# Kernel tuning notes

Hardware: AMD Instinct MI355X
Metric: run time of the kernel (lower is better)

The kernel has to match this reference:

```python
import jax, jax.numpy as jnp
import numpy as np

N = 50000      # nodes
E = 800000     # edges (avg degree 16)
D = 128        # feature / channel width (channel_counts=[128,128,128])
HEAD = 64      # head_dim
NEG_SLOPE = 0.2  # PyG GATConv leaky_relu slope


def setup_inputs() -> dict:
    key = jax.random.key(0)
    ks = jax.random.split(key, 32)
    s = 1.0 / np.sqrt(D)

    def w(k, shape):
        return jax.random.normal(k, shape, jnp.float32) * s

    return {
        "x": jax.random.normal(ks[0], (N, D), jnp.float32),
        "edge_index": jax.random.randint(ks[1], (2, E), 0, N, dtype=jnp.int32),
        # layer 0: lazy (-1,-1) GATConv -> separate src/dst linear maps
        "w0_src": w(ks[2], (D, D)), "w0_dst": w(ks[3], (D, D)),
        "a0_src": w(ks[4], (D,)), "a0_dst": w(ks[5], (D,)),
        "bc0": jnp.zeros((D,), jnp.float32),
        "wl0": w(ks[6], (D, D)), "bl0": jnp.zeros((D,), jnp.float32),
        # layer 1: int in_channels -> shared weight
        "w1": w(ks[7], (D, D)),
        "a1_src": w(ks[8], (D,)), "a1_dst": w(ks[9], (D,)),
        "bc1": jnp.zeros((D,), jnp.float32),
        "wl1": w(ks[10], (D, D)), "bl1": jnp.zeros((D,), jnp.float32),
        # layer 2
        "w2": w(ks[11], (D, D)),
        "a2_src": w(ks[12], (D,)), "a2_dst": w(ks[13], (D,)),
        "bc2": jnp.zeros((D,), jnp.float32),
        "wl2": w(ks[14], (D, D)), "bl2": jnp.zeros((D,), jnp.float32),
        # head linear
        "wh": w(ks[15], (D, HEAD)), "bh": jnp.zeros((HEAD,), jnp.float32),
    }


def _gat(h_src, h_dst, src, dst, a_src, a_dst, bias):
    """PyG GATConv (heads=1, no self loops, eval-mode). h_*: [N,C]."""
    al_s = h_src @ a_src                                   # [N]
    al_d = h_dst @ a_dst                                   # [N]
    logits = jax.nn.leaky_relu(al_s[src] + al_d[dst], NEG_SLOPE)  # [E]
    m = jax.ops.segment_max(logits, dst, num_segments=N)  # per-dest max
    e = jnp.exp(logits - m[dst])
    denom = jax.ops.segment_sum(e, dst, num_segments=N)
    alpha = e / denom[dst]                                 # [E]
    msg = h_src[src] * alpha[:, None]                      # [E,C]
    return jax.ops.segment_sum(msg, dst, num_segments=N) + bias


def reference(x, edge_index, w0_src, w0_dst, a0_src, a0_dst, bc0, wl0, bl0,
              w1, a1_src, a1_dst, bc1, wl1, bl1,
              w2, a2_src, a2_dst, bc2, wl2, bl2, wh, bh):
    src, dst = edge_index[0], edge_index[1]
    # layer 0: conv(x) + lin(x), relu
    h = _gat(x @ w0_src, x @ w0_dst, src, dst, a0_src, a0_dst, bc0) + x @ wl0 + bl0
    h = jax.nn.relu(h)
    # layer 1: shared-weight conv
    hs = h @ w1
    h = _gat(hs, hs, src, dst, a1_src, a1_dst, bc1) + h @ wl1 + bl1
    h = jax.nn.relu(h)
    # layer 2 (no relu)
    hs = h @ w2
    h = _gat(hs, hs, src, dst, a2_src, a2_dst, bc2) + h @ wl2 + bl2
    # head
    return h @ wh + bh
```

## Files before the change

kernel.cpp:

```cpp
#include <hip/hip_runtime.h>

#define NNODE 50000
#define NEDGE 800000
#define DIM   128
#define NEG   0.2f
#define NBUCK 196
#define EPB1  2048
#define NB1   391
#define GBLK  782

typedef __attribute__((ext_vector_type(8))) short bf16x8;
typedef __attribute__((ext_vector_type(4))) float f32x4;

__device__ __forceinline__ float wmax(float v){
  #pragma unroll
  for (int m = 32; m > 0; m >>= 1) v = fmaxf(v, __shfl_xor(v, m));
  return v;
}
__device__ __forceinline__ float wsum(float v){
  #pragma unroll
  for (int m = 32; m > 0; m >>= 1) v += __shfl_xor(v, m);
  return v;
}
__device__ __forceinline__ unsigned short f2bf(float f){
  unsigned int x = __float_as_uint(f);
  return (unsigned short)((x + 0x7fffu + ((x >> 16) & 1u)) >> 16);
}
__device__ __forceinline__ float bflo(unsigned u){ return __uint_as_float(u << 16); }
__device__ __forceinline__ float bfhi(unsigned u){ return __uint_as_float(u & 0xffff0000u); }

__global__ __launch_bounds__(256) void bhist2_k(const int* __restrict__ dst,
                                                int* __restrict__ cnt){
  __shared__ int h[NBUCK];
  for (int i = threadIdx.x; i < NBUCK; i += 256) h[i] = 0;
  __syncthreads();
  int e0 = blockIdx.x * EPB1 + threadIdx.x;
  #pragma unroll
  for (int i = 0; i < 8; ++i){
    int e = e0 + i * 256;
    if (e < NEDGE) atomicAdd(&h[dst[e] >> 8], 1);
  }
  __syncthreads();
  for (int i = threadIdx.x; i < NBUCK; i += 256)
    cnt[i * NB1 + blockIdx.x] = h[i];
}

__global__ __launch_bounds__(256) void scan196_k(const int* __restrict__ cnt,
                                                 int* __restrict__ cbase,
                                                 int* __restrict__ btot){
  __shared__ int sd[256];
  int b = blockIdx.x, t = threadIdx.x;
  const int* row = cnt + (size_t)b * NB1;
  int i0 = t * 2, i1 = t * 2 + 1;
  int v0 = (i0 < NB1) ? row[i0] : 0;
  int v1 = (i1 < NB1) ? row[i1] : 0;
  int s = v0 + v1;
  sd[t] = s; __syncthreads();
  #pragma unroll
  for (int off = 1; off < 256; off <<= 1){
    int u = (t >= off) ? sd[t - off] : 0;
    __syncthreads();
    sd[t] += u;
    __syncthreads();
  }
  int ex = sd[t] - s;
  if (i0 < NB1) cbase[(size_t)b * NB1 + i0] = ex;
  if (i1 < NB1) cbase[(size_t)b * NB1 + i1] = ex + v0;
  if (t == 255) btot[b] = sd[255];
}

__global__ __launch_bounds__(256) void bscan2_k(const int* __restrict__ btot,
                                                int* __restrict__ gbase,
                                                int* __restrict__ rp){
  __shared__ int sd[256];
  int t = threadIdx.x;
  int v = (t < NBUCK) ? btot[t] : 0;
  sd[t] = v; __syncthreads();
  #pragma unroll
  for (int off = 1; off < 256; off <<= 1){
    int u = (t >= off) ? sd[t - off] : 0;
    __syncthreads();
    sd[t] += u;
    __syncthreads();
  }
  if (t < NBUCK) gbase[t] = sd[t] - v;
  if (t == NBUCK - 1) gbase[NBUCK] = sd[t];
  if (t == 0) rp[NNODE] = NEDGE;
}

__global__ __launch_bounds__(256) void scat2_k(const int* __restrict__ ei,
                                               const int* __restrict__ gbase,
                                               const int* __restrict__ cbase,
                                               unsigned int* __restrict__ packed){
  __shared__ int lcur[NBUCK];
  for (int i = threadIdx.x; i < NBUCK; i += 256) lcur[i] = 0;
  __syncthreads();
  int e0 = blockIdx.x * EPB1 + threadIdx.x;
  #pragma unroll
  for (int i = 0; i < 8; ++i){
    int e = e0 + i * 256;
    if (e < NEDGE){
      int s = ei[e], d = ei[NEDGE + e];
      int b = d >> 8;
      int r = atomicAdd(&lcur[b], 1);
      int pos = gbase[b] + cbase[(size_t)b * NB1 + blockIdx.x] + r;
      packed[pos] = ((unsigned)d << 16) | (unsigned)s;
    }
  }
}

__global__ __launch_bounds__(256) void build_k(const int* __restrict__ gbase,
                                               const unsigned int* __restrict__ packed,
                                               int* __restrict__ rp,
                                               unsigned short* __restrict__ es){
  __shared__ int h[256], sd[256], cur[256];
  int b = blockIdx.x, t = threadIdx.x;
  int s0 = gbase[b], s1 = gbase[b + 1];
  h[t] = 0; __syncthreads();
  for (int i = s0 + t; i < s1; i += 256)
    atomicAdd(&h[(packed[i] >> 16) & 255], 1);
  __syncthreads();
  int v = h[t]; sd[t] = v; __syncthreads();
  #pragma unroll
  for (int off = 1; off < 256; off <<= 1){
    int u = (t >= off) ? sd[t - off] : 0;
    __syncthreads();
    sd[t] += u;
    __syncthreads();
  }
  int ex = sd[t] - v;
  cur[t] = ex;
  int d = b * 256 + t;
  if (d < NNODE) rp[d] = s0 + ex;
  __syncthreads();
  for (int i = s0 + t; i < s1; i += 256){
    unsigned int p = packed[i];
    int ld = (p >> 16) & 255;
    int pos = atomicAdd(&cur[ld], 1);
    es[s0 + pos] = (unsigned short)(p & 0xffffu);
  }
}

__global__ __launch_bounds__(256) void prepA_k(const float* __restrict__ w0s,
                                               const float* __restrict__ wl0,
                                               const float* __restrict__ w1,
                                               const float* __restrict__ wl1,
                                               unsigned short* __restrict__ Wz1,
                                               unsigned short* __restrict__ Wz2){
  int g = blockIdx.x * 256 + threadIdx.x;
  int layer = g >> 12;
  int rem = g & 4095;
  int ct = rem >> 9, q = (rem >> 6) & 7, lane = rem & 63;
  int quad = lane >> 4;
  int c = ct * 16 + (lane & 15);
  const float* wA = layer ? w1 : w0s;
  const float* wB = layer ? wl1 : wl0;
  unsigned short* dst = (layer ? Wz2 : Wz1) + ((size_t)(ct * 8 + q) * 64 + lane) * 8;
  #pragma unroll
  for (int j = 0; j < 8; ++j){
    int k = q * 32 + quad * 8 + j;
    float v = (k < 128) ? wA[k * 128 + c] : wB[(k - 128) * 128 + c];
    dst[j] = f2bf(v);
  }
}

__global__ __launch_bounds__(256) void prepH_k(const float* __restrict__ w2,
                                               const float* __restrict__ wl2,
                                               const float* __restrict__ wh,
                                               const float* __restrict__ bc2,
                                               const float* __restrict__ bl2,
                                               const float* __restrict__ bh,
                                               unsigned short* __restrict__ Wz3,
                                               float* __restrict__ bf3){
  if (blockIdx.x == 8){
    int c = threadIdx.x;
    if (c < 64){
      float s = bh[c];
      for (int t = 0; t < 128; ++t) s += (bc2[t] + bl2[t]) * wh[t * 64 + c];
      bf3[c] = s;
    }
    return;
  }
  int g = blockIdx.x * 256 + threadIdx.x;
  int ct = g >> 9, q = (g >> 6) & 7, lane = g & 63;
  int quad = lane >> 4;
  int c = ct * 16 + (lane & 15);
  unsigned short* dst = Wz3 + ((size_t)(ct * 8 + q) * 64 + lane) * 8;
  #pragma unroll
  for (int j = 0; j < 8; ++j){
    int k = q * 32 + quad * 8 + j;
    const float* src = (k < 128) ? (w2 + k * 128) : (wl2 + (k - 128) * 128);
    float s = 0.f;
    for (int t = 0; t < 128; ++t) s += src[t] * wh[t * 64 + c];
    dst[j] = f2bf(s);
  }
}

__global__ void mv6_k(const float* __restrict__ w0s, const float* __restrict__ a0s,
                      const float* __restrict__ w0d, const float* __restrict__ a0d,
                      const float* __restrict__ w1,  const float* __restrict__ a1s,
                      const float* __restrict__ a1d,
                      const float* __restrict__ w2,  const float* __restrict__ a2s,
                      const float* __restrict__ a2d,
                      const float* __restrict__ bc0, const float* __restrict__ bl0,
                      const float* __restrict__ bc1, const float* __restrict__ bl1,
                      float* __restrict__ uv,
                      float* __restrict__ bf1, float* __restrict__ bf2){
  if (blockIdx.x == 192){
    int t = threadIdx.x;
    if (t < 128) bf1[t] = bc0[t] + bl0[t];
    else bf2[t - 128] = bc1[t - 128] + bl1[t - 128];
    return;
  }
  int lane = threadIdx.x & 63;
  int idx = blockIdx.x * 4 + (threadIdx.x >> 6);
  int grp = idx >> 7, r = idx & 127;
  const float* W; const float* a;
  switch (grp){
    case 0: W = w0s; a = a0s; break;
    case 1: W = w0d; a = a0d; break;
    case 2: W = w1;  a = a1s; break;
    case 3: W = w1;  a = a1d; break;
    case 4: W = w2;  a = a2s; break;
    default: W = w2; a = a2d; break;
  }
  float2 w = ((const float2*)(W + r * DIM))[lane];
  float2 av = ((const float2*)a)[lane];
  float s = wsum(w.x * av.x + w.y * av.y);
  if (lane == 0) uv[grp * 128 + r] = s;
}

__global__ __launch_bounds__(256) void cvtdual_k(const float* __restrict__ X,
                                                 const float* __restrict__ uv,
                                                 unsigned int* __restrict__ Xb,
                                                 float* __restrict__ als,
                                                 float* __restrict__ ald){
  int lane = threadIdx.x & 63;
  int n = blockIdx.x * 4 + (threadIdx.x >> 6);
  if (n >= NNODE) return;
  float2 xv = ((const float2*)(X + (size_t)n * DIM))[lane];
  Xb[(size_t)n * 64 + lane] = (unsigned)f2bf(xv.x) | ((unsigned)f2bf(xv.y) << 16);
  float2 uu = ((const float2*)uv)[lane];
  float2 vv = ((const float2*)(uv + 128))[lane];
  float s1 = wsum(xv.x * uu.x + xv.y * uu.y);
  float s2 = wsum(xv.x * vv.x + xv.y * vv.y);
  if (lane == 0){ als[n] = s1; ald[n] = s2; }
}

__global__ __launch_bounds__(256) void gat_k(const int* __restrict__ rp,
                                             const unsigned short* __restrict__ es,
                                             const float* __restrict__ als,
                                             const float* __restrict__ ald,
                                             const unsigned int* __restrict__ A,
                                             unsigned int* __restrict__ Mb){
  int lane = threadIdx.x & 63;
  int n = blockIdx.x * 4 + (threadIdx.x >> 6);
  if (n >= NNODE) return;
  int start = rp[n], end = rp[n + 1];
  int deg = end - start;
  float ad = ald[n];
  float2 acc = make_float2(0.f, 0.f);
  float rinv = 0.f;

  if (deg <= 64){
    int s = 0; float z = -3.0e38f;
    if (lane < deg){
      s = es[start + lane];
      float t = als[s] + ad;
      z = t > 0.f ? t : NEG * t;
    }
    float m = wmax(z);
    float e = (lane < deg) ? __expf(z - m) : 0.f;
    float denom = wsum(e);
    rinv = (deg > 0) ? 1.f / denom : 0.f;
    int dq = (deg + 7) & ~7;
    for (int j = 0; j < dq; j += 8){
      int   s0 = __shfl(s, j),     s1 = __shfl(s, j + 1);
      int   s2 = __shfl(s, j + 2), s3 = __shfl(s, j + 3);
      int   s4 = __shfl(s, j + 4), s5 = __shfl(s, j + 5);
      int   s6 = __shfl(s, j + 6), s7 = __shfl(s, j + 7);
      float w0 = __shfl(e, j),     w1 = __shfl(e, j + 1);
      float w2 = __shfl(e, j + 2), w3 = __shfl(e, j + 3);
      float w4 = __shfl(e, j + 4), w5 = __shfl(e, j + 5);
      float w6 = __shfl(e, j + 6), w7 = __shfl(e, j + 7);
      unsigned p0 = A[(size_t)s0 * 64 + lane];
      unsigned p1 = A[(size_t)s1 * 64 + lane];
      unsigned p2 = A[(size_t)s2 * 64 + lane];
      unsigned p3 = A[(size_t)s3 * 64 + lane];
      unsigned p4 = A[(size_t)s4 * 64 + lane];
      unsigned p5 = A[(size_t)s5 * 64 + lane];
      unsigned p6 = A[(size_t)s6 * 64 + lane];
      unsigned p7 = A[(size_t)s7 * 64 + lane];
      acc.x = fmaf(w0, bflo(p0), acc.x); acc.y = fmaf(w0, bfhi(p0), acc.y);
      acc.x = fmaf(w1, bflo(p1), acc.x); acc.y = fmaf(w1, bfhi(p1), acc.y);
      acc.x = fmaf(w2, bflo(p2), acc.x); acc.y = fmaf(w2, bfhi(p2), acc.y);
      acc.x = fmaf(w3, bflo(p3), acc.x); acc.y = fmaf(w3, bfhi(p3), acc.y);
      acc.x = fmaf(w4, bflo(p4), acc.x); acc.y = fmaf(w4, bfhi(p4), acc.y);
      acc.x = fmaf(w5, bflo(p5), acc.x); acc.y = fmaf(w5, bfhi(p5), acc.y);
      acc.x = fmaf(w6, bflo(p6), acc.x); acc.y = fmaf(w6, bfhi(p6), acc.y);
      acc.x = fmaf(w7, bflo(p7), acc.x); acc.y = fmaf(w7, bfhi(p7), acc.y);
    }
  } else {
    float mloc = -3.0e38f;
    for (int i = start + lane; i < end; i += 64){
      int s = es[i];
      float zz = als[s] + ad;
      zz = zz > 0.f ? zz : NEG * zz;
      mloc = fmaxf(mloc, zz);
    }
    float m = wmax(mloc);
    float dloc = 0.f;
    for (int i = start + lane; i < end; i += 64){
      int s = es[i];
      float zz = als[s] + ad;
      zz = zz > 0.f ? zz : NEG * zz;
      dloc += __expf(zz - m);
    }
    rinv = 1.f / wsum(dloc);
    for (int i = start; i < end; ++i){
      int s = es[i];
      float zz = als[s] + ad;
      zz = zz > 0.f ? zz : NEG * zz;
      float w = __expf(zz - m);
      unsigned p = A[(size_t)s * 64 + lane];
      acc.x = fmaf(w, bflo(p), acc.x);
      acc.y = fmaf(w, bfhi(p), acc.y);
    }
  }

  Mb[(size_t)n * 64 + lane] =
      (unsigned)f2bf(acc.x * rinv) | ((unsigned)f2bf(acc.y * rinv) << 16);
}

template<int FINAL>
__global__ __launch_bounds__(256) void mfma_k(const unsigned int* __restrict__ Mb,
                                              const unsigned int* __restrict__ Hin,
                                              const unsigned short* __restrict__ Wz,
                                              const float* __restrict__ bias,
                                              const float* __restrict__ u,
                                              const float* __restrict__ v,
                                              unsigned short* __restrict__ Hout,
                                              float* __restrict__ outf,
                                              float* __restrict__ als,
                                              float* __restrict__ ald){
  int lane = threadIdx.x & 63;
  int wid  = threadIdx.x >> 6;
  int r0   = blockIdx.x * 64 + wid * 16;
  int quad = lane >> 4;
  int col  = lane & 15;

  int rA = r0 + col; if (rA > NNODE - 1) rA = NNODE - 1;
  const bf16x8* mrow = (const bf16x8*)(Mb + (size_t)rA * 64);
  const bf16x8* hrow = (const bf16x8*)(Hin + (size_t)rA * 64);
  bf16x8 a[8];
  #pragma unroll
  for (int q = 0; q < 4; ++q){
    a[q]     = mrow[q * 4 + quad];
    a[q + 4] = hrow[q * 4 + quad];
  }

  const bf16x8* wz = (const bf16x8*)Wz;
  int rowq = r0 + quad * 4;
  float alsp[4] = {0.f, 0.f, 0.f, 0.f};
  float aldp[4] = {0.f, 0.f, 0.f, 0.f};
  const int NCT = FINAL ? 4 : 8;

  #pragma unroll
  for (int ct = 0; ct < NCT; ++ct){
    f32x4 acc = {0.f, 0.f, 0.f, 0.f};
    #pragma unroll
    for (int q = 0; q < 8; ++q){
      bf16x8 bfr = wz[(ct * 8 + q) * 64 + lane];
      acc = __builtin_amdgcn_mfma_f32_16x16x32_bf16(a[q], bfr, acc, 0, 0, 0);
    }
    int c = ct * 16 + col;
    float bb = bias[c];
    if (FINAL){
      #pragma unroll
      for (int r = 0; r < 4; ++r){
        int row = rowq + r;
        if (row < NNODE) outf[(size_t)row * 64 + c] = acc[r] + bb;
      }
    } else {
      float uc = u[c], vc = v[c];
      #pragma unroll
      for (int r = 0; r < 4; ++r){
        float h = fmaxf(acc[r] + bb, 0.f);
        alsp[r] = fmaf(h, uc, alsp[r]);
        aldp[r] = fmaf(h, vc, aldp[r]);
        int row = rowq + r;
        if (row < NNODE) Hout[(size_t)row * 128 + c] = f2bf(h);
      }
    }
  }

  if (!FINAL){
    #pragma unroll
    for (int m = 1; m < 16; m <<= 1){
      #pragma unroll
      for (int r = 0; r < 4; ++r){
        alsp[r] += __shfl_xor(alsp[r], m);
        aldp[r] += __shfl_xor(aldp[r], m);
      }
    }
    if (col == 0){
      #pragma unroll
      for (int r = 0; r < 4; ++r){
        int row = rowq + r;
        if (row < NNODE){ als[row] = alsp[r]; ald[row] = aldp[r]; }
      }
    }
  }
}

extern "C" void kernel_launch(void* const* d_in, const int* in_sizes, int n_in,
                              void* d_out, int out_size, void* d_ws, size_t ws_size,
                              hipStream_t stream){
  const float* x   = (const float*)d_in[0];
  const int*   ei  = (const int*)d_in[1];
  const float* w0s = (const float*)d_in[2];
  const float* w0d = (const float*)d_in[3];
  const float* a0s = (const float*)d_in[4];
  const float* a0d = (const float*)d_in[5];
  const float* bc0 = (const float*)d_in[6];
  const float* wl0 = (const float*)d_in[7];
  const float* bl0 = (const float*)d_in[8];
  const float* w1  = (const float*)d_in[9];
  const float* a1s = (const float*)d_in[10];
  const float* a1d = (const float*)d_in[11];
  const float* bc1 = (const float*)d_in[12];
  const float* wl1 = (const float*)d_in[13];
  const float* bl1 = (const float*)d_in[14];
  const float* w2  = (const float*)d_in[15];
  const float* a2s = (const float*)d_in[16];
  const float* a2d = (const float*)d_in[17];
  const float* bc2 = (const float*)d_in[18];
  const float* wl2 = (const float*)d_in[19];
  const float* bl2 = (const float*)d_in[20];
  const float* wh  = (const float*)d_in[21];
  const float* bh  = (const float*)d_in[22];
  float* out = (float*)d_out;

  unsigned int* Mb = (unsigned int*)d_ws;
  unsigned int* Xb = Mb + (size_t)NNODE * 64;
  unsigned int* Ha = Xb + (size_t)NNODE * 64;
  unsigned int* Hb = Ha + (size_t)NNODE * 64;
  float* als  = (float*)(Hb + (size_t)NNODE * 64);
  float* ald  = als + NNODE;
  float* uv   = ald + NNODE;
  float* bf1  = uv + 6 * 128;
  float* bf2  = bf1 + 128;
  float* bf3  = bf2 + 128;
  unsigned short* Wz1 = (unsigned short*)(bf3 + 64);
  unsigned short* Wz2 = Wz1 + 256 * 128;
  unsigned short* Wz3 = Wz2 + 256 * 128;
  int*   rp    = (int*)(Wz3 + 256 * 64);
  int*   cnt   = rp + (NNODE + 1);
  int*   cbase = cnt + NBUCK * NB1;
  int*   btot  = cbase + NBUCK * NB1;
  int*   gbase = btot + NBUCK;
  unsigned int* packed = (unsigned int*)(gbase + (NBUCK + 1));
  unsigned short* es   = (unsigned short*)(packed + NEDGE);

  bhist2_k<<<NB1, 256, 0, stream>>>(ei + NEDGE, cnt);
  scan196_k<<<NBUCK, 256, 0, stream>>>(cnt, cbase, btot);
  bscan2_k<<<1, 256, 0, stream>>>(btot, gbase, rp);
  scat2_k<<<NB1, 256, 0, stream>>>(ei, gbase, cbase, packed);
  build_k<<<NBUCK, 256, 0, stream>>>(gbase, packed, rp, es);

  dim3 b(256);
  dim3 gn((NNODE + 3) / 4);

  prepA_k<<<32, b, 0, stream>>>(w0s, wl0, w1, wl1, Wz1, Wz2);
  prepH_k<<<9, b, 0, stream>>>(w2, wl2, wh, bc2, bl2, bh, Wz3, bf3);
  mv6_k<<<193, b, 0, stream>>>(w0s, a0s, w0d, a0d, w1, a1s, a1d, w2, a2s, a2d,
                               bc0, bl0, bc1, bl1, uv, bf1, bf2);
  cvtdual_k<<<gn, b, 0, stream>>>(x, uv, Xb, als, ald);

  gat_k<<<gn, b, 0, stream>>>(rp, es, als, ald, Xb, Mb);
  mfma_k<0><<<GBLK, b, 0, stream>>>(Mb, Xb, Wz1, bf1, uv + 2 * 128, uv + 3 * 128,
                                    (unsigned short*)Ha, nullptr, als, ald);

  gat_k<<<gn, b, 0, stream>>>(rp, es, als, ald, Ha, Mb);
  mfma_k<0><<<GBLK, b, 0, stream>>>(Mb, Ha, Wz2, bf2, uv + 4 * 128, uv + 5 * 128,
                                    (unsigned short*)Hb, nullptr, als, ald);

  gat_k<<<gn, b, 0, stream>>>(rp, es, als, ald, Hb, Mb);
  mfma_k<1><<<GBLK, b, 0, stream>>>(Mb, Hb, Wz3, bf3, nullptr, nullptr,
                                    nullptr, out, nullptr, nullptr);
}
```

Before: 330.5 us.

## Fuse GAT aggregation with MFMA linear into one kernel per layer

```diff
diff --git a/kernel.cpp b/kernel.cpp
--- a/kernel.cpp
+++ b/kernel.cpp
@@ -8,6 +8,7 @@
 #define EPB1  2048
 #define NB1   391
 #define GBLK  782
+#define MSTR  136
 
 typedef __attribute__((ext_vector_type(8))) short bf16x8;
 typedef __attribute__((ext_vector_type(4))) float f32x4;
@@ -247,120 +248,118 @@
   if (lane == 0){ als[n] = s1; ald[n] = s2; }
 }
 
-__global__ __launch_bounds__(256) void gat_k(const int* __restrict__ rp,
-                                             const unsigned short* __restrict__ es,
-                                             const float* __restrict__ als,
-                                             const float* __restrict__ ald,
-                                             const unsigned int* __restrict__ A,
-                                             unsigned int* __restrict__ Mb){
+template<int FINAL>
+__global__ __launch_bounds__(256) void gm_k(const int* __restrict__ rp,
+                                            const unsigned short* __restrict__ es,
+                                            const float* __restrict__ als_in,
+                                            const float* __restrict__ ald_in,
+                                            const unsigned int* __restrict__ Hg,
+                                            const unsigned short* __restrict__ Wz,
+                                            const float* __restrict__ bias,
+                                            const float* __restrict__ u,
+                                            const float* __restrict__ v,
+                                            unsigned short* __restrict__ Hout,
+                                            float* __restrict__ outf,
+                                            float* __restrict__ als_out,
+                                            float* __restrict__ ald_out){
+  __shared__ unsigned short Ms[64 * MSTR + 8];
   int lane = threadIdx.x & 63;
-  int n = blockIdx.x * 4 + (threadIdx.x >> 6);
-  if (n >= NNODE) return;
-  int start = rp[n], end = rp[n + 1];
-  int deg = end - start;
-  float ad = ald[n];
-  float2 acc = make_float2(0.f, 0.f);
-  float rinv = 0.f;
-
-  if (deg <= 64){
-    int s = 0; float z = -3.0e38f;
-    if (lane < deg){
-      s = es[start + lane];
-      float t = als[s] + ad;
-      z = t > 0.f ? t : NEG * t;
-    }
-    float m = wmax(z);
-    float e = (lane < deg) ? __expf(z - m) : 0.f;
-    float denom = wsum(e);
-    rinv = (deg > 0) ? 1.f / denom : 0.f;
-    int dq = (deg + 7) & ~7;
-    for (int j = 0; j < dq; j += 8){
-      int   s0 = __shfl(s, j),     s1 = __shfl(s, j + 1);
-      int   s2 = __shfl(s, j + 2), s3 = __shfl(s, j + 3);
-      int   s4 = __shfl(s, j + 4), s5 = __shfl(s, j + 5);
-      int   s6 = __shfl(s, j + 6), s7 = __shfl(s, j + 7);
-      float w0 = __shfl(e, j),     w1 = __shfl(e, j + 1);
-      float w2 = __shfl(e, j + 2), w3 = __shfl(e, j + 3);
-      float w4 = __shfl(e, j + 4), w5 = __shfl(e, j + 5);
-      float w6 = __shfl(e, j + 6), w7 = __shfl(e, j + 7);
-      unsigned p0 = A[(size_t)s0 * 64 + lane];
-      unsigned p1 = A[(size_t)s1 * 64 + lane];
-      unsigned p2 = A[(size_t)s2 * 64 + lane];
-      unsigned p3 = A[(size_t)s3 * 64 + lane];
-      unsigned p4 = A[(size_t)s4 * 64 + lane];
-      unsigned p5 = A[(size_t)s5 * 64 + lane];
-      unsigned p6 = A[(size_t)s6 * 64 + lane];
-      unsigned p7 = A[(size_t)s7 * 64 + lane];
-      acc.x = fmaf(w0, bflo(p0), acc.x); acc.y = fmaf(w0, bfhi(p0), acc.y);
-      acc.x = fmaf(w1, bflo(p1), acc.x); acc.y = fmaf(w1, bfhi(p1), acc.y);
-      acc.x = fmaf(w2, bflo(p2), acc.x); acc.y = fmaf(w2, bfhi(p2), acc.y);
-      acc.x = fmaf(w3, bflo(p3), acc.x); acc.y = fmaf(w3, bfhi(p3), acc.y);
-      acc.x = fmaf(w4, bflo(p4), acc.x); acc.y = fmaf(w4, bfhi(p4), acc.y);
-      acc.x = fmaf(w5, bflo(p5), acc.x); acc.y = fmaf(w5, bfhi(p5), acc.y);
-      acc.x = fmaf(w6, bflo(p6), acc.x); acc.y = fmaf(w6, bfhi(p6), acc.y);
-      acc.x = fmaf(w7, bflo(p7), acc.x); acc.y = fmaf(w7, bfhi(p7), acc.y);
-    }
-  } else {
-    float mloc = -3.0e38f;
-    for (int i = start + lane; i < end; i += 64){
-      int s = es[i];
-      float zz = als[s] + ad;
-      zz = zz > 0.f ? zz : NEG * zz;
-      mloc = fmaxf(mloc, zz);
-    }
-    float m = wmax(mloc);
-    float dloc = 0.f;
-    for (int i = start + lane; i < end; i += 64){
-      int s = es[i];
-      float zz = als[s] + ad;
-      zz = zz > 0.f ? zz : NEG * zz;
-      dloc += __expf(zz - m);
-    }
-    rinv = 1.f / wsum(dloc);
-    for (int i = start; i < end; ++i){
-      int s = es[i];
-      float zz = als[s] + ad;
-      zz = zz > 0.f ? zz : NEG * zz;
-      float w = __expf(zz - m);
-      unsigned p = A[(size_t)s * 64 + lane];
-      acc.x = fmaf(w, bflo(p), acc.x);
-      acc.y = fmaf(w, bfhi(p), acc.y);
-    }
-  }
-
-  Mb[(size_t)n * 64 + lane] =
-      (unsigned)f2bf(acc.x * rinv) | ((unsigned)f2bf(acc.y * rinv) << 16);
-}
-
-template<int FINAL>
-__global__ __launch_bounds__(256) void mfma_k(const unsigned int* __restrict__ Mb,
-                                              const unsigned int* __restrict__ Hin,
-                                              const unsigned short* __restrict__ Wz,
-                                              const float* __restrict__ bias,
-                                              const float* __restrict__ u,
-                                              const float* __restrict__ v,
-                                              unsigned short* __restrict__ Hout,
-                                              float* __restrict__ outf,
-                                              float* __restrict__ als,
-                                              float* __restrict__ ald){
-  int lane = threadIdx.x & 63;
-  int wid  = threadIdx.x >> 6;
-  int r0   = blockIdx.x * 64 + wid * 16;
+  int wave = threadIdx.x >> 6;
+  int r0w  = blockIdx.x * 64 + wave * 16;
+
+  for (int i = 0; i < 16; ++i){
+    int n = r0w + i;
+    float2 acc = make_float2(0.f, 0.f);
+    float rinv = 0.f;
+    if (n < NNODE){
+      int start = rp[n], end = rp[n + 1];
+      int deg = end - start;
+      float ad = ald_in[n];
+      if (deg <= 64){
+        int s = 0; float z = -3.0e38f;
+        if (lane < deg){
+          s = es[start + lane];
+          float t = als_in[s] + ad;
+          z = t > 0.f ? t : NEG * t;
+        }
+        float m = wmax(z);
+        float e = (lane < deg) ? __expf(z - m) : 0.f;
+        float denom = wsum(e);
+        rinv = (deg > 0) ? 1.f / denom : 0.f;
+        int dq = (deg + 7) & ~7;
+        for (int j = 0; j < dq; j += 8){
+          int   s0 = __shfl(s, j),     s1 = __shfl(s, j + 1);
+          int   s2 = __shfl(s, j + 2), s3 = __shfl(s, j + 3);
+          int   s4 = __shfl(s, j + 4), s5 = __shfl(s, j + 5);
+          int   s6 = __shfl(s, j + 6), s7 = __shfl(s, j + 7);
+          float w0 = __shfl(e, j),     w1 = __shfl(e, j + 1);
+          float w2 = __shfl(e, j + 2), w3 = __shfl(e, j + 3);
+          float w4 = __shfl(e, j + 4), w5 = __shfl(e, j + 5);
+          float w6 = __shfl(e, j + 6), w7 = __shfl(e, j + 7);
+          unsigned p0 = Hg[(size_t)s0 * 64 + lane];
+          unsigned p1 = Hg[(size_t)s1 * 64 + lane];
+          unsigned p2 = Hg[(size_t)s2 * 64 + lane];
+          unsigned p3 = Hg[(size_t)s3 * 64 + lane];
+          unsigned p4 = Hg[(size_t)s4 * 64 + lane];
+          unsigned p5 = Hg[(size_t)s5 * 64 + lane];
+          unsigned p6 = Hg[(size_t)s6 * 64 + lane];
+          unsigned p7 = Hg[(size_t)s7 * 64 + lane];
+          acc.x = fmaf(w0, bflo(p0), acc.x); acc.y = fmaf(w0, bfhi(p0), acc.y);
+          acc.x = fmaf(w1, bflo(p1), acc.x); acc.y = fmaf(w1, bfhi(p1), acc.y);
+          acc.x = fmaf(w2, bflo(p2), acc.x); acc.y = fmaf(w2, bfhi(p2), acc.y);
+          acc.x = fmaf(w3, bflo(p3), acc.x); acc.y = fmaf(w3, bfhi(p3), acc.y);
+          acc.x = fmaf(w4, bflo(p4), acc.x); acc.y = fmaf(w4, bfhi(p4), acc.y);
+          acc.x = fmaf(w5, bflo(p5), acc.x); acc.y = fmaf(w5, bfhi(p5), acc.y);
+          acc.x = fmaf(w6, bflo(p6), acc.x); acc.y = fmaf(w6, bfhi(p6), acc.y);
+          acc.x = fmaf(w7, bflo(p7), acc.x); acc.y = fmaf(w7, bfhi(p7), acc.y);
+        }
+      } else {
+        float mloc = -3.0e38f;
+        for (int ii = start + lane; ii < end; ii += 64){
+          int s = es[ii];
+          float zz = als_in[s] + ad;
+          zz = zz > 0.f ? zz : NEG * zz;
+          mloc = fmaxf(mloc, zz);
+        }
+        float m = wmax(mloc);
+        float dloc = 0.f;
+        for (int ii = start + lane; ii < end; ii += 64){
+          int s = es[ii];
+          float zz = als_in[s] + ad;
+          zz = zz > 0.f ? zz : NEG * zz;
+          dloc += __expf(zz - m);
+        }
+        rinv = 1.f / wsum(dloc);
+        for (int ii = start; ii < end; ++ii){
+          int s = es[ii];
+          float zz = als_in[s] + ad;
+          zz = zz > 0.f ? zz : NEG * zz;
+          float w = __expf(zz - m);
+          unsigned p = Hg[(size_t)s * 64 + lane];
+          acc.x = fmaf(w, bflo(p), acc.x);
+          acc.y = fmaf(w, bfhi(p), acc.y);
+        }
+      }
+    }
+    int nl = wave * 16 + i;
+    *(unsigned*)&Ms[nl * MSTR + lane * 2] =
+        (unsigned)f2bf(acc.x * rinv) | ((unsigned)f2bf(acc.y * rinv) << 16);
+  }
+  __syncthreads();
+
   int quad = lane >> 4;
   int col  = lane & 15;
-
-  int rA = r0 + col; if (rA > NNODE - 1) rA = NNODE - 1;
-  const bf16x8* mrow = (const bf16x8*)(Mb + (size_t)rA * 64);
-  const bf16x8* hrow = (const bf16x8*)(Hin + (size_t)rA * 64);
+  int rA = r0w + col; if (rA > NNODE - 1) rA = NNODE - 1;
+  const bf16x8* hrow = (const bf16x8*)(Hg + (size_t)rA * 64);
   bf16x8 a[8];
   #pragma unroll
   for (int q = 0; q < 4; ++q){
-    a[q]     = mrow[q * 4 + quad];
+    a[q]     = *(const bf16x8*)&Ms[(wave * 16 + col) * MSTR + q * 32 + quad * 8];
     a[q + 4] = hrow[q * 4 + quad];
   }
 
   const bf16x8* wz = (const bf16x8*)Wz;
-  int rowq = r0 + quad * 4;
+  int rowq = r0w + quad * 4;
   float alsp[4] = {0.f, 0.f, 0.f, 0.f};
   float aldp[4] = {0.f, 0.f, 0.f, 0.f};
   const int NCT = FINAL ? 4 : 8;
@@ -407,7 +406,7 @@
       #pragma unroll
       for (int r = 0; r < 4; ++r){
         int row = rowq + r;
-        if (row < NNODE){ als[row] = alsp[r]; ald[row] = aldp[r]; }
+        if (row < NNODE){ als_out[row] = alsp[r]; ald_out[row] = aldp[r]; }
       }
     }
   }
@@ -441,13 +440,14 @@
   const float* bh  = (const float*)d_in[22];
   float* out = (float*)d_out;
 
-  unsigned int* Mb = (unsigned int*)d_ws;
-  unsigned int* Xb = Mb + (size_t)NNODE * 64;
+  unsigned int* Xb = (unsigned int*)d_ws;
   unsigned int* Ha = Xb + (size_t)NNODE * 64;
   unsigned int* Hb = Ha + (size_t)NNODE * 64;
-  float* als  = (float*)(Hb + (size_t)NNODE * 64);
-  float* ald  = als + NNODE;
-  float* uv   = ald + NNODE;
+  float* alsA = (float*)(Hb + (size_t)NNODE * 64);
+  float* aldA = alsA + NNODE;
+  float* alsB = aldA + NNODE;
+  float* aldB = alsB + NNODE;
+  float* uv   = aldB + NNODE;
   float* bf1  = uv + 6 * 128;
   float* bf2  = bf1 + 128;
   float* bf3  = bf2 + 128;
@@ -475,17 +475,17 @@
   prepH_k<<<9, b, 0, stream>>>(w2, wl2, wh, bc2, bl2, bh, Wz3, bf3);
   mv6_k<<<193, b, 0, stream>>>(w0s, a0s, w0d, a0d, w1, a1s, a1d, w2, a2s, a2d,
                                bc0, bl0, bc1, bl1, uv, bf1, bf2);
-  cvtdual_k<<<gn, b, 0, stream>>>(x, uv, Xb, als, ald);
-
-  gat_k<<<gn, b, 0, stream>>>(rp, es, als, ald, Xb, Mb);
-  mfma_k<0><<<GBLK, b, 0, stream>>>(Mb, Xb, Wz1, bf1, uv + 2 * 128, uv + 3 * 128,
-                                    (unsigned short*)Ha, nullptr, als, ald);
-
-  gat_k<<<gn, b, 0, stream>>>(rp, es, als, ald, Ha, Mb);
-  mfma_k<0><<<GBLK, b, 0, stream>>>(Mb, Ha, Wz2, bf2, uv + 4 * 128, uv + 5 * 128,
-                                    (unsigned short*)Hb, nullptr, als, ald);
-
-  gat_k<<<gn, b, 0, stream>>>(rp, es, als, ald, Hb, Mb);
-  mfma_k<1><<<GBLK, b, 0, stream>>>(Mb, Hb, Wz3, bf3, nullptr, nullptr,
-                                    nullptr, out, nullptr, nullptr);
-}
+  cvtdual_k<<<gn, b, 0, stream>>>(x, uv, Xb, alsA, aldA);
+
+  gm_k<0><<<GBLK, b, 0, stream>>>(rp, es, alsA, aldA, Xb, Wz1, bf1,
+                                  uv + 2 * 128, uv + 3 * 128,
+                                  (unsigned short*)Ha, nullptr, alsB, aldB);
+
+  gm_k<0><<<GBLK, b, 0, stream>>>(rp, es, alsB, aldB, Ha, Wz2, bf2,
+                                  uv + 4 * 128, uv + 5 * 128,
+                                  (unsigned short*)Hb, nullptr, alsA, aldA);
+
+  gm_k<1><<<GBLK, b, 0, stream>>>(rp, es, alsA, aldA, Hb, Wz3, bf3,
+                                  nullptr, nullptr, nullptr, out,
+                                  nullptr, nullptr);
+}
```

After: 366.6 us. 10.9% more time.
